# Kernel optimization log

Hardware: AMD Instinct MI355X
Metric: run time of the kernel (lower is better)

## Reference

```python
import jax, jax.numpy as jnp
import numpy as np

B, S, HID = 2, 4096, 768
H, DH = 12, 64
FF = 3072
W = 128  # one-sided attention band; window span = 2*W+1
EPS = 1e-12


def _ln(x, g, b):
    m = jnp.mean(x, axis=-1, keepdims=True)
    v = jnp.var(x, axis=-1, keepdims=True)
    return (x - m) * jax.lax.rsqrt(v + EPS) * g + b


def _band_attend(q, k, v, dmask, w):
    # q,k,v: (B,H,S,D) fp32; dmask: (B,S,2w+1) additive key-mask. Returns (B,S,H,D).
    b, h, s, d = q.shape
    nc = s // w
    qc = q.reshape(b, h, nc, w, d)
    pad = ((0, 0), (0, 0), (w, w), (0, 0))
    kp = jnp.pad(k, pad)
    vp = jnp.pad(v, pad)
    win = jnp.arange(nc)[:, None] * w + jnp.arange(3 * w)[None, :]  # (nc, 3w) indices into padded seq
    kc = kp[:, :, win]  # (B,H,nc,3w,D)
    vc = vp[:, :, win]
    s3 = jnp.einsum('bhcxd,bhcyd->bhcxy', qc, kc)  # (B,H,nc,w,3w)
    # extract band: query i in chunk attends keys j in [i, i+2w] of the 3w window
    off = jnp.arange(w)[:, None] + jnp.arange(2 * w + 1)[None, :]  # (w, 2w+1)
    band = jnp.take_along_axis(s3, off[None, None, None], axis=-1)  # (B,H,nc,w,2w+1)
    band = band.reshape(b, h, s, 2 * w + 1)
    keypos = jnp.arange(s)[:, None] + jnp.arange(-w, w + 1)[None, :]
    valid = (keypos >= 0) & (keypos < s)  # mask_invalid_locations
    band = jnp.where(valid[None, None], band, -1e30)
    band = band + dmask[:, None]
    p = jax.nn.softmax(band, axis=-1)
    # scatter probs back to chunk-dense (w, 3w) layout for the PV matmul
    pc = p.reshape(b, h, nc, w, 2 * w + 1)
    j = jnp.arange(3 * w)[None, :] - jnp.arange(w)[:, None]  # (w,3w) offset indices
    ok = (j >= 0) & (j <= 2 * w)
    jcl = jnp.clip(j, 0, 2 * w)
    pdense = jnp.take_along_axis(pc, jcl[None, None, None], axis=-1)  # (B,H,nc,w,3w)
    pdense = jnp.where(ok[None, None, None], pdense, 0.0)
    ctx = jnp.einsum('bhcxy,bhcyd->bhcxd', pdense, vc)  # (B,H,nc,w,D)
    return ctx.reshape(b, h, s, d).transpose(0, 2, 1, 3)


def setup_inputs() -> dict:
    key = jax.random.key(0)
    ks = jax.random.split(key, 8)
    sc = 0.02
    inp = {
        'hidden_states': jax.random.normal(ks[0], (B, S, HID), jnp.float32),
        'attention_mask': jax.random.randint(ks[1], (B, 1, 1, S), 0, 2, jnp.int32),
        'Wq': jax.random.normal(ks[2], (HID, HID), jnp.float32) * sc,
        'bq': jnp.zeros((HID,), jnp.float32),
        'Wk': jax.random.normal(ks[3], (HID, HID), jnp.float32) * sc,
        'bk': jnp.zeros((HID,), jnp.float32),
        'Wv': jax.random.normal(ks[4], (HID, HID), jnp.float32) * sc,
        'bv': jnp.zeros((HID,), jnp.float32),
        'Wd': jax.random.normal(ks[5], (HID, HID), jnp.float32) * sc,
        'bd': jnp.zeros((HID,), jnp.float32),
        'ln1_g': jnp.ones((HID,), jnp.float32),
        'ln1_b': jnp.zeros((HID,), jnp.float32),
        'Wf': jax.random.normal(ks[6], (HID, FF), jnp.float32) * sc,
        'bf': jnp.zeros((FF,), jnp.float32),
        'Wo': jax.random.normal(ks[7], (FF, HID), jnp.float32) * sc,
        'bo': jnp.zeros((HID,), jnp.float32),
        'ln2_g': jnp.ones((HID,), jnp.float32),
        'ln2_b': jnp.zeros((HID,), jnp.float32),
    }
    return inp


def reference(hidden_states, attention_mask, Wq, bq, Wk, bk, Wv, bv, Wd, bd,
              ln1_g, ln1_b, Wf, bf, Wo, bo, ln2_g, ln2_b):
    def heads(x):
        return x.reshape(B, S, H, DH).transpose(0, 2, 1, 3)  # (B,H,S,DH)

    q = heads(hidden_states @ Wq + bq).astype(jnp.float32) / np.float32(np.sqrt(DH))
    k = heads(hidden_states @ Wk + bk).astype(jnp.float32)
    v = heads(hidden_states @ Wv + bv).astype(jnp.float32)

    am = attention_mask.reshape(B, S)
    maskvals = jnp.where(am != 0, -10000.0, 0.0).astype(jnp.float32)  # (B,S)
    mpad = jnp.pad(maskvals, ((0, 0), (W, W)))
    kidx = jnp.arange(S)[:, None] + jnp.arange(2 * W + 1)[None, :]
    dmask = mpad[:, kidx]  # (B,S,2w+1)

    ctx = _band_attend(q, k, v, dmask, W)  # (B,S,H,DH)

    w_d = Wd.reshape(H, DH, HID)
    proj = jnp.einsum('bfnd,ndh->bfh', ctx, w_d) + bd
    attn_out = _ln(hidden_states + proj, ln1_g, ln1_b)

    ff = jax.nn.gelu(attn_out @ Wf + bf, approximate=False)
    ff = ff @ Wo + bo
    return _ln(ff + attn_out, ln2_g, ln2_b)
```

## Files before the change

kernel.cpp:

```cpp
#include <hip/hip_runtime.h>
#include <cstdint>
#include <cstddef>

#define S_LEN 4096
#define HIDD 768
#define NH 12
#define FFD 3072

typedef float f32x4 __attribute__((ext_vector_type(4)));
typedef short s16x8 __attribute__((ext_vector_type(8)));
typedef short s16x4 __attribute__((ext_vector_type(4)));

__device__ __forceinline__ short f2bf(float f) {
  unsigned u = __float_as_uint(f);
  u += 0x7fffu + ((u >> 16) & 1u);
  return (short)(u >> 16);
}
__device__ __forceinline__ float bf2f(short s) {
  return __uint_as_float(((unsigned)(unsigned short)s) << 16);
}

__device__ __forceinline__ void gload16(const short* g, short* l) {
  __builtin_amdgcn_global_load_lds(
      (__attribute__((address_space(1))) void*)(void*)const_cast<short*>(g),
      (__attribute__((address_space(3))) void*)l, 16, 0, 0);
}

__global__ void prep_k(const float* __restrict__ x, short* __restrict__ xo,
                       const float* __restrict__ Wq, const float* __restrict__ Wk,
                       const float* __restrict__ Wv, const float* __restrict__ Wd,
                       const float* __restrict__ Wf, const float* __restrict__ Wo,
                       short* __restrict__ oq, short* __restrict__ ok_,
                       short* __restrict__ ov, short* __restrict__ od,
                       short* __restrict__ of_, short* __restrict__ oo) {
  __shared__ float tl[64][65];
  int id = blockIdx.x;
  if (id < 6144) {
    size_t i = (size_t)id * 256 + threadIdx.x;
    float4 f = ((const float4*)x)[i];
    s16x4 v;
    v[0] = f2bf(f.x); v[1] = f2bf(f.y); v[2] = f2bf(f.z); v[3] = f2bf(f.w);
    ((s16x4*)xo)[i] = v;
    return;
  }
  id -= 6144;
  const float* in; short* out; int R, C, tr, tc;
  if (id < 576) {
    int wsel = id / 144; int t = id % 144; tr = t / 12; tc = t % 12; R = 768; C = 768;
    in = wsel == 0 ? Wq : wsel == 1 ? Wk : wsel == 2 ? Wv : Wd;
    out = wsel == 0 ? oq : wsel == 1 ? ok_ : wsel == 2 ? ov : od;
  } else if (id < 1152) {
    int t = id - 576; tr = t / 48; tc = t % 48; R = 768; C = 3072; in = Wf; out = of_;
  } else {
    int t = id - 1152; tr = t / 12; tc = t % 12; R = 3072; C = 768; in = Wo; out = oo;
  }
  int r0 = tr * 64, c0 = tc * 64;
  int tid = threadIdx.x;
  #pragma unroll
  for (int i = 0; i < 16; i++) {
    int idx = i * 256 + tid; int r = idx >> 6, cc = idx & 63;
    tl[r][cc] = in[(size_t)(r0 + r) * C + c0 + cc];
  }
  __syncthreads();
  #pragma unroll
  for (int i = 0; i < 16; i++) {
    int idx = i * 256 + tid; int cc = idx >> 6, rr = idx & 63;
    out[(size_t)(c0 + cc) * R + r0 + rr] = f2bf(tl[rr][cc]);
  }
}

template <int EPI, int BN>
__global__ void __launch_bounds__(256) gemm_bt(
    const short* __restrict__ A, const short* __restrict__ Bt,
    const float* __restrict__ bias, const float* __restrict__ bias1,
    const float* __restrict__ bias2, const void* __restrict__ resid,
    void* __restrict__ out, int N, int K) {
  constexpr int NT = BN / 32;
  __shared__ __align__(16) short As[2][128 * 64];
  __shared__ __align__(16) short Bs[2][BN * 64];
  const int tid = threadIdx.x;
  const int lane = tid & 63;
  const int w = tid >> 6;
  const int wr = w >> 1, wc = w & 1;
  const int m0 = blockIdx.x * 128, n0 = blockIdx.y * BN;
  const int lr = lane >> 3;
  const int seg = (lane & 7) ^ lr;
  f32x4 acc[4][NT];
  #pragma unroll
  for (int i = 0; i < 4; i++)
    #pragma unroll
    for (int j = 0; j < NT; j++) { acc[i][j][0] = 0.f; acc[i][j][1] = 0.f; acc[i][j][2] = 0.f; acc[i][j][3] = 0.f; }

  const short* Ab = A + (size_t)(m0 + lr) * K + seg * 8;
  const short* Bb = Bt + (size_t)(n0 + lr) * K + seg * 8;

  auto stage = [&](int buf, int k0) {
    #pragma unroll
    for (int i = 0; i < 4; i++) {
      const int ca = w * 4 + i;
      gload16(Ab + (size_t)(ca * 8) * K + k0, &As[buf][ca * 512]);
    }
    #pragma unroll
    for (int i = 0; i < NT; i++) {
      const int cb = w * NT + i;
      gload16(Bb + (size_t)(cb * 8) * K + k0, &Bs[buf][cb * 512]);
    }
  };

  const int nt_k = K >> 6;
  stage(0, 0);
  __syncthreads();
  int cur = 0;
  for (int t = 0; t < nt_k; ++t) {
    if (t + 1 < nt_k) stage(cur ^ 1, (t + 1) << 6);
    const int kc = (lane >> 4) * 8;
    #pragma unroll
    for (int ks = 0; ks < 2; ks++) {
      const int kb = ks * 32 + kc;
      s16x8 af[4], bfr[NT];
      #pragma unroll
      for (int mt = 0; mt < 4; mt++) {
        const int arow = wr * 64 + mt * 16 + (lane & 15);
        af[mt] = *(const s16x8*)&As[cur][arow * 64 + (kb ^ ((arow & 7) << 3))];
      }
      #pragma unroll
      for (int nt = 0; nt < NT; nt++) {
        const int brow = wc * (BN / 2) + nt * 16 + (lane & 15);
        bfr[nt] = *(const s16x8*)&Bs[cur][brow * 64 + (kb ^ ((brow & 7) << 3))];
      }
      #pragma unroll
      for (int mt = 0; mt < 4; mt++)
        #pragma unroll
        for (int nt = 0; nt < NT; nt++)
          acc[mt][nt] = __builtin_amdgcn_mfma_f32_16x16x32_bf16(af[mt], bfr[nt], acc[mt][nt], 0, 0, 0);
    }
    if (t + 1 < nt_k) { __syncthreads(); cur ^= 1; }
  }
  #pragma unroll
  for (int nt = 0; nt < NT; nt++) {
    const int col = n0 + wc * (BN / 2) + nt * 16 + (lane & 15);
    if (EPI == 0) {
      const int cwhich = col >= 1536 ? 2 : (col >= 768 ? 1 : 0);
      const int cwi = col - cwhich * 768;
      const float* bsel = cwhich == 0 ? bias : (cwhich == 1 ? bias1 : bias2);
      const float bvv = bsel[cwi];
      const int hh = cwi >> 6, dh = cwi & 63;
      if (cwhich == 2) {
        short* vtp = (short*)resid;
        #pragma unroll
        for (int mt = 0; mt < 4; mt++) {
          const int row = m0 + wr * 64 + mt * 16 + (lane >> 4) * 4;
          const int b = row >> 12, s = row & 4095;
          s16x4 o;
          #pragma unroll
          for (int rr = 0; rr < 4; rr++) o[rr] = f2bf(acc[mt][nt][rr] + bvv);
          *(s16x4*)&vtp[(((size_t)(b * NH + hh) * 64 + dh) << 12) + s] = o;
        }
      } else {
        const float sc = (cwhich == 0) ? 0.125f : 1.f;
        short* outp = (short*)out + (size_t)cwhich * ((size_t)8192 * 768);
        #pragma unroll
        for (int mt = 0; mt < 4; mt++) {
          #pragma unroll
          for (int rr = 0; rr < 4; rr++) {
            const int row = m0 + wr * 64 + mt * 16 + (lane >> 4) * 4 + rr;
            const int b = row >> 12, s = row & 4095;
            outp[((((size_t)b * NH + hh) * S_LEN + s) << 6) + dh] = f2bf((acc[mt][nt][rr] + bvv) * sc);
          }
        }
      }
    } else {
      const float bvv = bias[col];
      #pragma unroll
      for (int mt = 0; mt < 4; mt++) {
        #pragma unroll
        for (int rr = 0; rr < 4; rr++) {
          const int row = m0 + wr * 64 + mt * 16 + (lane >> 4) * 4 + rr;
          float v = acc[mt][nt][rr] + bvv;
          if (EPI == 1) {
            float u = 0.7978845608f * v * (1.f + 0.044715f * v * v);
            float e = __expf(2.f * u);
            float th = 1.f - 2.f / (e + 1.f);
            ((short*)out)[(size_t)row * N + col] = f2bf(0.5f * v * (1.f + th));
          } else if (EPI == 2) {
            ((float*)out)[(size_t)row * N + col] = v + ((const float*)resid)[(size_t)row * N + col];
          } else {
            ((float*)out)[(size_t)row * N + col] = v + bf2f(((const short*)resid)[(size_t)row * N + col]);
          }
        }
      }
    }
  }
}

__global__ void __launch_bounds__(512, 1) attn_k(
    const short* __restrict__ qh, const short* __restrict__ kh,
    const short* __restrict__ vth, const int* __restrict__ am,
    short* __restrict__ ctx) {
  extern __shared__ char smraw[];
  short* Kb = (short*)smraw;
  float* dmw = (float*)(smraw + 55296);
  short* Pb = (short*)(smraw + 56832);
  const int c = blockIdx.x;
  const int bh = blockIdx.y;
  const int b = bh / NH, hh = bh % NH;
  const int tid = threadIdx.x, lane = tid & 63, w = tid >> 6;
  const int q0 = c * 128, kw0 = q0 - 128;

  for (int ch = tid; ch < 3072; ch += 512) {
    int n = ch >> 3, seg = ch & 7;
    int kp = kw0 + n; kp = kp < 0 ? 0 : (kp > S_LEN - 1 ? S_LEN - 1 : kp);
    *(s16x8*)&Kb[n * 72 + seg * 8] = *(const s16x8*)&kh[(((size_t)bh * S_LEN + kp) << 6) + seg * 8];
  }
  for (int n = tid; n < 384; n += 512) {
    int kp = kw0 + n;
    float d;
    if (kp < 0 || kp >= S_LEN) d = -1e30f;
    else d = (am[b * S_LEN + kp] != 0) ? -10000.f : 0.f;
    dmw[n] = d;
  }
  __syncthreads();

  const short* qrow = qh + ((((size_t)bh * S_LEN) + q0 + w * 16 + (lane & 15)) << 6);
  s16x8 aq0 = *(const s16x8*)&qrow[(lane >> 4) * 8];
  s16x8 aq1 = *(const s16x8*)&qrow[32 + (lane >> 4) * 8];

  f32x4 sacc[24];
  #pragma unroll
  for (int t = 0; t < 24; t++) { sacc[t][0] = 0.f; sacc[t][1] = 0.f; sacc[t][2] = 0.f; sacc[t][3] = 0.f; }
  #pragma unroll
  for (int t = 0; t < 24; t++) {
    const short* kr = &Kb[(t * 16 + (lane & 15)) * 72 + (lane >> 4) * 8];
    s16x8 bk0 = *(const s16x8*)&kr[0];
    s16x8 bk1 = *(const s16x8*)&kr[32];
    sacc[t] = __builtin_amdgcn_mfma_f32_16x16x32_bf16(aq0, bk0, sacc[t], 0, 0, 0);
    sacc[t] = __builtin_amdgcn_mfma_f32_16x16x32_bf16(aq1, bk1, sacc[t], 0, 0, 0);
  }
  const int mbase = w * 16 + (lane >> 4) * 4;
  #pragma unroll
  for (int t = 0; t < 24; t++) {
    int n = t * 16 + (lane & 15);
    float d = dmw[n];
    #pragma unroll
    for (int r = 0; r < 4; r++) {
      int j = n - (mbase + r);
      float sv = sacc[t][r] + d;
      if (j < 0 || j > 256) sv = -1e30f;
      sacc[t][r] = sv;
    }
  }
  short* Pw = Pb + w * 16 * 392;
  #pragma unroll
  for (int r = 0; r < 4; r++) {
    float mx = -3e38f;
    #pragma unroll
    for (int t = 0; t < 24; t++) mx = fmaxf(mx, sacc[t][r]);
    #pragma unroll
    for (int d = 1; d < 16; d <<= 1) mx = fmaxf(mx, __shfl_xor(mx, d));
    float sum = 0.f;
    #pragma unroll
    for (int t = 0; t < 24; t++) { float p = __expf(sacc[t][r] - mx); sacc[t][r] = p; sum += p; }
    #pragma unroll
    for (int d = 1; d < 16; d <<= 1) sum += __shfl_xor(sum, d);
    float inv = 1.f / sum;
    #pragma unroll
    for (int t = 0; t < 24; t++)
      Pw[((lane >> 4) * 4 + r) * 392 + t * 16 + (lane & 15)] = f2bf(sacc[t][r] * inv);
  }
  __syncthreads();

  short* Vt = (short*)smraw;
  for (int ch = tid; ch < 3072; ch += 512) {
    int dh = ch / 48, seg = ch % 48;
    int n0 = seg * 8, kp0 = kw0 + n0;
    const short* vr = vth + (((size_t)bh * 64 + dh) << 12);
    s16x8 vv;
    if (kp0 >= 0 && kp0 + 7 < S_LEN) {
      vv = *(const s16x8*)&vr[kp0];
    } else {
      #pragma unroll
      for (int e = 0; e < 8; e++) {
        int kp = kp0 + e; kp = kp < 0 ? 0 : (kp > S_LEN - 1 ? S_LEN - 1 : kp);
        vv[e] = vr[kp];
      }
    }
    *(s16x8*)&Vt[dh * 392 + n0] = vv;
  }
  __syncthreads();

  f32x4 oacc[4];
  #pragma unroll
  for (int i = 0; i < 4; i++) { oacc[i][0] = 0.f; oacc[i][1] = 0.f; oacc[i][2] = 0.f; oacc[i][3] = 0.f; }
  #pragma unroll
  for (int ksp = 0; ksp < 12; ksp++) {
    s16x8 pa = *(const s16x8*)&Pw[(lane & 15) * 392 + ksp * 32 + (lane >> 4) * 8];
    #pragma unroll
    for (int ct = 0; ct < 4; ct++) {
      s16x8 vb = *(const s16x8*)&Vt[(ct * 16 + (lane & 15)) * 392 + ksp * 32 + (lane >> 4) * 8];
      oacc[ct] = __builtin_amdgcn_mfma_f32_16x16x32_bf16(pa, vb, oacc[ct], 0, 0, 0);
    }
  }
  #pragma unroll
  for (int ct = 0; ct < 4; ct++) {
    #pragma unroll
    for (int r = 0; r < 4; r++) {
      int srow = q0 + w * 16 + (lane >> 4) * 4 + r;
      int col = hh * 64 + ct * 16 + (lane & 15);
      ctx[((size_t)b * S_LEN + srow) * HIDD + col] = f2bf(oacc[ct][r]);
    }
  }
}

template <int OUTBF>
__global__ void ln_k(const float* __restrict__ in, const float* __restrict__ g,
                     const float* __restrict__ bb, void* __restrict__ out) {
  int row = blockIdx.x * 4 + (threadIdx.x >> 6);
  int lane = threadIdx.x & 63;
  const float4* x = (const float4*)(in + (size_t)row * HIDD);
  float4 v0 = x[lane], v1 = x[lane + 64], v2 = x[lane + 128];
  float s = v0.x + v0.y + v0.z + v0.w + v1.x + v1.y + v1.z + v1.w + v2.x + v2.y + v2.z + v2.w;
  float ss = v0.x * v0.x + v0.y * v0.y + v0.z * v0.z + v0.w * v0.w
           + v1.x * v1.x + v1.y * v1.y + v1.z * v1.z + v1.w * v1.w
           + v2.x * v2.x + v2.y * v2.y + v2.z * v2.z + v2.w * v2.w;
  #pragma unroll
  for (int d = 1; d < 64; d <<= 1) { s += __shfl_xor(s, d); ss += __shfl_xor(ss, d); }
  float mean = s * (1.f / 768.f);
  float var = ss * (1.f / 768.f) - mean * mean;
  float rs = rsqrtf(var + 1e-12f);
  const float4* gp = (const float4*)g;
  const float4* bp = (const float4*)bb;
  #pragma unroll
  for (int seg = 0; seg < 3; seg++) {
    int idx = lane + seg * 64;
    float4 vv = seg == 0 ? v0 : seg == 1 ? v1 : v2;
    float4 gg = gp[idx], b4 = bp[idx];
    float o0 = (vv.x - mean) * rs * gg.x + b4.x;
    float o1 = (vv.y - mean) * rs * gg.y + b4.y;
    float o2 = (vv.z - mean) * rs * gg.z + b4.z;
    float o3 = (vv.w - mean) * rs * gg.w + b4.w;
    if (OUTBF) {
      s16x4 o; o[0] = f2bf(o0); o[1] = f2bf(o1); o[2] = f2bf(o2); o[3] = f2bf(o3);
      ((s16x4*)out)[(size_t)row * 192 + idx] = o;
    } else {
      float4 o; o.x = o0; o.y = o1; o.z = o2; o.w = o3;
      ((float4*)out)[(size_t)row * 192 + idx] = o;
    }
  }
}

extern "C" void kernel_launch(void* const* d_in, const int* in_sizes, int n_in,
                              void* d_out, int out_size, void* d_ws, size_t ws_size,
                              hipStream_t stream) {
  const float* hid = (const float*)d_in[0];
  const int* am = (const int*)d_in[1];
  const float* Wq = (const float*)d_in[2];  const float* bq = (const float*)d_in[3];
  const float* Wk = (const float*)d_in[4];  const float* bk = (const float*)d_in[5];
  const float* Wv = (const float*)d_in[6];  const float* bv = (const float*)d_in[7];
  const float* Wd = (const float*)d_in[8];  const float* bd = (const float*)d_in[9];
  const float* g1 = (const float*)d_in[10]; const float* b1 = (const float*)d_in[11];
  const float* Wf = (const float*)d_in[12]; const float* bf = (const float*)d_in[13];
  const float* Wo = (const float*)d_in[14]; const float* bo = (const float*)d_in[15];
  const float* g2 = (const float*)d_in[16]; const float* b2 = (const float*)d_in[17];

  char* ws = (char*)d_ws;
  size_t off = 0;
  auto alloc = [&](size_t bytes) { char* p = ws + off; off += (bytes + 255) & ~(size_t)255; return p; };
  short* Xb   = (short*)alloc((size_t)8192 * 768 * 2);
  short* Wqb  = (short*)alloc((size_t)768 * 768 * 2);
  short* Wkb  = (short*)alloc((size_t)768 * 768 * 2);
  short* Wvb  = (short*)alloc((size_t)768 * 768 * 2);
  short* Wdb  = (short*)alloc((size_t)768 * 768 * 2);
  short* Wfb  = (short*)alloc((size_t)3072 * 768 * 2);
  short* Wob  = (short*)alloc((size_t)768 * 3072 * 2);
  short* qh   = (short*)alloc((size_t)8192 * 768 * 2);
  short* kh   = (short*)alloc((size_t)8192 * 768 * 2);
  short* vth  = (short*)alloc((size_t)8192 * 768 * 2);
  short* ctx  = (short*)alloc((size_t)8192 * 768 * 2);
  short* aob  = (short*)alloc((size_t)8192 * 768 * 2);
  short* ffb  = (short*)alloc((size_t)8192 * 3072 * 2);
  float* f2r  = (float*)alloc((size_t)8192 * 768 * 4);
  float* ln1in = (float*)d_out;
  (void)kh;

  hipFuncSetAttribute(reinterpret_cast<const void*>(attn_k),
                      hipFuncAttributeMaxDynamicSharedMemorySize, 157184);

  prep_k<<<7872, 256, 0, stream>>>(hid, Xb, Wq, Wk, Wv, Wd, Wf, Wo,
                                   Wqb, Wkb, Wvb, Wdb, Wfb, Wob);

  gemm_bt<0, 128><<<dim3(64, 18), 256, 0, stream>>>(Xb, Wqb, bq, bk, bv, vth, qh, 2304, 768);
  attn_k<<<dim3(32, 24), 512, 157184, stream>>>(qh, kh, vth, am, ctx);
  gemm_bt<2, 64><<<dim3(64, 12), 256, 0, stream>>>(ctx, Wdb, bd, nullptr, nullptr, hid, ln1in, 768, 768);
  ln_k<1><<<2048, 256, 0, stream>>>(ln1in, g1, b1, aob);
  gemm_bt<1, 128><<<dim3(64, 24), 256, 0, stream>>>(aob, Wfb, bf, nullptr, nullptr, nullptr, ffb, 3072, 768);
  gemm_bt<3, 64><<<dim3(64, 12), 256, 0, stream>>>(ffb, Wob, bo, nullptr, nullptr, aob, f2r, 768, 3072);
  ln_k<0><<<2048, 256, 0, stream>>>(f2r, g2, b2, d_out);
}
```

Measured before the change: 256.1 us.

## Overlap GEMM prefetch with compute via vmcnt waits; move V transpose to separate kernel

The GEMM main loop replaces the __syncthreads barriers with an explicit partial s_waitcnt vmcnt and raw s_barrier. The current tile can then be consumed while the next tile's global_load_lds is still in flight, hiding load latency. The QKV epilogue now writes V in the same head-major layout as Q/K, and a new vtrans_k kernel transposes V into the (b,h,d,s) layout attention expects. This removes the strided scattered V stores in the GEMM epilogue at the cost of an extra launch and a round trip of V through memory. The vmcnt counts are hand-tuned to the number of loads per stage and are fragile if the staging changes.

Result: no change. 259.8 us (+1.4%).

```diff
diff --git a/kernel.cpp b/kernel.cpp
--- a/kernel.cpp
+++ b/kernel.cpp
@@ -66,6 +66,25 @@
   for (int i = 0; i < 16; i++) {
     int idx = i * 256 + tid; int cc = idx >> 6, rr = idx & 63;
     out[(size_t)(c0 + cc) * R + r0 + rr] = f2bf(tl[rr][cc]);
+  }
+}
+
+__global__ void vtrans_k(const short* __restrict__ vh, short* __restrict__ vth) {
+  __shared__ short tl[64][72];
+  int s0 = blockIdx.x * 64; int bh = blockIdx.y;
+  int tid = threadIdx.x;
+  const short* base = vh + ((size_t)bh << 18);
+  #pragma unroll
+  for (int i = 0; i < 16; i++) {
+    int idx = i * 256 + tid; int r = idx >> 6, cc = idx & 63;
+    tl[r][cc] = base[(size_t)(s0 + r) * 64 + cc];
+  }
+  __syncthreads();
+  short* ob = vth + ((size_t)bh << 18);
+  #pragma unroll
+  for (int i = 0; i < 16; i++) {
+    int idx = i * 256 + tid; int dh = idx >> 6, s = idx & 63;
+    ob[((size_t)dh << 12) + s0 + s] = tl[s][dh];
   }
 }
 
@@ -109,10 +128,18 @@
 
   const int nt_k = K >> 6;
   stage(0, 0);
-  __syncthreads();
   int cur = 0;
   for (int t = 0; t < nt_k; ++t) {
-    if (t + 1 < nt_k) stage(cur ^ 1, (t + 1) << 6);
+    const bool more = (t + 1 < nt_k);
+    if (more) stage(cur ^ 1, (t + 1) << 6);
+    if (more) {
+      if constexpr (NT == 4) asm volatile("s_waitcnt vmcnt(8)" ::: "memory");
+      else                   asm volatile("s_waitcnt vmcnt(6)" ::: "memory");
+    } else {
+      asm volatile("s_waitcnt vmcnt(0)" ::: "memory");
+    }
+    __builtin_amdgcn_s_barrier();
+    __builtin_amdgcn_sched_barrier(0);
     const int kc = (lane >> 4) * 8;
     #pragma unroll
     for (int ks = 0; ks < 2; ks++) {
@@ -134,7 +161,11 @@
         for (int nt = 0; nt < NT; nt++)
           acc[mt][nt] = __builtin_amdgcn_mfma_f32_16x16x32_bf16(af[mt], bfr[nt], acc[mt][nt], 0, 0, 0);
     }
-    if (t + 1 < nt_k) { __syncthreads(); cur ^= 1; }
+    if (more) {
+      __builtin_amdgcn_sched_barrier(0);
+      __builtin_amdgcn_s_barrier();
+      cur ^= 1;
+    }
   }
   #pragma unroll
   for (int nt = 0; nt < NT; nt++) {
@@ -144,29 +175,16 @@
       const int cwi = col - cwhich * 768;
       const float* bsel = cwhich == 0 ? bias : (cwhich == 1 ? bias1 : bias2);
       const float bvv = bsel[cwi];
+      const float sc = (cwhich == 0) ? 0.125f : 1.f;
       const int hh = cwi >> 6, dh = cwi & 63;
-      if (cwhich == 2) {
-        short* vtp = (short*)resid;
+      short* outp = (short*)out + (size_t)cwhich * ((size_t)8192 * 768);
+      #pragma unroll
+      for (int mt = 0; mt < 4; mt++) {
         #pragma unroll
-        for (int mt = 0; mt < 4; mt++) {
-          const int row = m0 + wr * 64 + mt * 16 + (lane >> 4) * 4;
+        for (int rr = 0; rr < 4; rr++) {
+          const int row = m0 + wr * 64 + mt * 16 + (lane >> 4) * 4 + rr;
           const int b = row >> 12, s = row & 4095;
-          s16x4 o;
-          #pragma unroll
-          for (int rr = 0; rr < 4; rr++) o[rr] = f2bf(acc[mt][nt][rr] + bvv);
-          *(s16x4*)&vtp[(((size_t)(b * NH + hh) * 64 + dh) << 12) + s] = o;
-        }
-      } else {
-        const float sc = (cwhich == 0) ? 0.125f : 1.f;
-        short* outp = (short*)out + (size_t)cwhich * ((size_t)8192 * 768);
-        #pragma unroll
-        for (int mt = 0; mt < 4; mt++) {
-          #pragma unroll
-          for (int rr = 0; rr < 4; rr++) {
-            const int row = m0 + wr * 64 + mt * 16 + (lane >> 4) * 4 + rr;
-            const int b = row >> 12, s = row & 4095;
-            outp[((((size_t)b * NH + hh) * S_LEN + s) << 6) + dh] = f2bf((acc[mt][nt][rr] + bvv) * sc);
-          }
+          outp[((((size_t)b * NH + hh) * S_LEN + s) << 6) + dh] = f2bf((acc[mt][nt][rr] + bvv) * sc);
         }
       }
     } else {
@@ -374,13 +392,14 @@
   short* Wob  = (short*)alloc((size_t)768 * 3072 * 2);
   short* qh   = (short*)alloc((size_t)8192 * 768 * 2);
   short* kh   = (short*)alloc((size_t)8192 * 768 * 2);
+  short* vh   = (short*)alloc((size_t)8192 * 768 * 2);
   short* vth  = (short*)alloc((size_t)8192 * 768 * 2);
   short* ctx  = (short*)alloc((size_t)8192 * 768 * 2);
   short* aob  = (short*)alloc((size_t)8192 * 768 * 2);
   short* ffb  = (short*)alloc((size_t)8192 * 3072 * 2);
   float* f2r  = (float*)alloc((size_t)8192 * 768 * 4);
   float* ln1in = (float*)d_out;
-  (void)kh;
+  (void)kh; (void)vh;
 
   hipFuncSetAttribute(reinterpret_cast<const void*>(attn_k),
                       hipFuncAttributeMaxDynamicSharedMemorySize, 157184);
@@ -388,7 +407,8 @@
   prep_k<<<7872, 256, 0, stream>>>(hid, Xb, Wq, Wk, Wv, Wd, Wf, Wo,
                                    Wqb, Wkb, Wvb, Wdb, Wfb, Wob);
 
-  gemm_bt<0, 128><<<dim3(64, 18), 256, 0, stream>>>(Xb, Wqb, bq, bk, bv, vth, qh, 2304, 768);
+  gemm_bt<0, 128><<<dim3(64, 18), 256, 0, stream>>>(Xb, Wqb, bq, bk, bv, nullptr, qh, 2304, 768);
+  vtrans_k<<<dim3(64, 24), 256, 0, stream>>>(vh, vth);
   attn_k<<<dim3(32, 24), 512, 157184, stream>>>(qh, kh, vth, am, ctx);
   gemm_bt<2, 64><<<dim3(64, 12), 256, 0, stream>>>(ctx, Wdb, bd, nullptr, nullptr, hid, ln1in, 768, 768);
   ln_k<1><<<2048, 256, 0, stream>>>(ln1in, g1, b1, aob);
```
